# Performance work log

Hardware: AMD Instinct MI355X
Metric: run time of the kernel (lower is better)

## Reference

```python
import jax, jax.numpy as jnp
import numpy as np

N = 50000      # nodes
E = 800000     # edges (avg degree 16)
D_IN = 128     # node_feature_dim
H = 256        # hidden_dim
EPS = 1e-5     # BatchNorm eps


def setup_inputs() -> dict:
    key = jax.random.key(0)
    ks = jax.random.split(key, 32)
    inp = {
        "x": jax.random.normal(ks[0], (N, D_IN), jnp.float32),
        "edge_index": jax.random.randint(ks[1], (2, E), 0, N, jnp.int32),
    }
    dims = [(D_IN, H), (H, H), (H, H)]
    k = 2
    for i, (din, dout) in enumerate(dims):
        s = 1.0 / np.sqrt(din)
        inp[f"Wl{i}"] = jax.random.uniform(ks[k], (din, dout), jnp.float32, -s, s); k += 1
        inp[f"bl{i}"] = jax.random.uniform(ks[k], (dout,), jnp.float32, -s, s); k += 1
        inp[f"Wr{i}"] = jax.random.uniform(ks[k], (din, dout), jnp.float32, -s, s); k += 1
        inp[f"g{i}"] = jnp.ones((dout,), jnp.float32)
        inp[f"b{i}"] = jnp.zeros((dout,), jnp.float32)
        inp[f"rm{i}"] = jax.random.normal(ks[k], (dout,), jnp.float32) * 0.1; k += 1
        inp[f"rv{i}"] = jax.random.uniform(ks[k], (dout,), jnp.float32, 0.5, 1.5); k += 1
    return inp


def _sage(x, src, dst, Wl, bl, Wr):
    # PyG SAGEConv (aggr='mean'): out = lin_l(mean_{j in N(i)} x_j) + lin_r(x_i)
    deg = jax.ops.segment_sum(jnp.ones((src.shape[0],), x.dtype), dst, num_segments=N)
    agg = jax.ops.segment_sum(x[src], dst, num_segments=N)  # [N, d_in]
    mean = agg / jnp.maximum(deg, 1.0)[:, None]
    return mean @ Wl + bl + x @ Wr


def _bn(x, g, b, rm, rv):
    # eval-mode BatchNorm1d with running stats
    return (x - rm) * (g * jax.lax.rsqrt(rv + EPS)) + b


def reference(x, edge_index,
              Wl0, bl0, Wr0, g0, b0, rm0, rv0,
              Wl1, bl1, Wr1, g1, b1, rm1, rv1,
              Wl2, bl2, Wr2, g2, b2, rm2, rv2):
    src, dst = edge_index[0], edge_index[1]
    h = jax.nn.relu(_bn(_sage(x, src, dst, Wl0, bl0, Wr0), g0, b0, rm0, rv0))
    h = jax.nn.relu(_bn(_sage(h, src, dst, Wl1, bl1, Wr1), g1, b1, rm1, rv1))
    h = _bn(_sage(h, src, dst, Wl2, bl2, Wr2), g2, b2, rm2, rv2)
    return h  # [N, H] node embeddings (dropout is identity in eval mode)
```

## Files before the change

kernel.cpp:

```cpp
#include <hip/hip_runtime.h>
#include <hip/hip_bf16.h>

#define NNODES 50000
#define NEDGES 800000
#define HID 256
#define BN_EPS 1e-5f
#define SCAN_B ((NNODES + 255) / 256)

typedef __attribute__((ext_vector_type(8))) short short8v;
typedef __attribute__((ext_vector_type(4))) float f32x4;
typedef __attribute__((ext_vector_type(2))) float f32x2;

__device__ inline void load_lds16(const void* g, void* l) {
    __builtin_amdgcn_global_load_lds(
        (const __attribute__((address_space(1))) unsigned int*)g,
        (__attribute__((address_space(3))) unsigned int*)l, 16, 0, 0);
}

__global__ void k_countrank(const int* __restrict__ ei, int* __restrict__ cnt,
                            int* __restrict__ rank, int nE) {
    int e = blockIdx.x * blockDim.x + threadIdx.x;
    if (e < nE) rank[e] = atomicAdd(&cnt[ei[nE + e]], 1);
}

__global__ void k_bsum(const int* __restrict__ cnt, int* __restrict__ loc,
                       int* __restrict__ bsum, int n) {
    __shared__ int sh[256];
    int tid = threadIdx.x;
    int i = blockIdx.x * 256 + tid;
    int v = (i < n) ? cnt[i] : 0;
    sh[tid] = v;
    __syncthreads();
    for (int off = 1; off < 256; off <<= 1) {
        int t = (tid >= off) ? sh[tid - off] : 0;
        __syncthreads();
        sh[tid] += t;
        __syncthreads();
    }
    if (i < n) loc[i] = sh[tid] - v;
    if (tid == 255) bsum[blockIdx.x] = sh[255];
}

__global__ void k_bscan(int* __restrict__ bsum, int nb) {
    __shared__ int sh[256];
    int tid = threadIdx.x;
    int v = (tid < nb) ? bsum[tid] : 0;
    sh[tid] = v;
    __syncthreads();
    for (int off = 1; off < 256; off <<= 1) {
        int t = (tid >= off) ? sh[tid - off] : 0;
        __syncthreads();
        sh[tid] += t;
        __syncthreads();
    }
    if (tid < nb) bsum[tid] = sh[tid] - v;
}

__global__ void k_addoff(const int* __restrict__ loc, const int* __restrict__ bsum,
                         int* __restrict__ rowptr, int n, int nE) {
    int i = blockIdx.x * 256 + threadIdx.x;
    if (i < n) rowptr[i] = loc[i] + bsum[blockIdx.x];
    if (i == 0) rowptr[n] = nE;
}

__global__ void k_fill2(const int* __restrict__ ei, const int* __restrict__ rowptr,
                        const int* __restrict__ rank, int* __restrict__ col, int nE) {
    int e = blockIdx.x * blockDim.x + threadIdx.x;
    if (e < nE) col[rowptr[ei[nE + e]] + rank[e]] = ei[e];
}

#define PREP_CAST 1600000
#define PREP_TR   327680
__global__ void k_prep(const float* __restrict__ x,
                       __hip_bfloat16* __restrict__ xb, unsigned char* __restrict__ x8,
                       const float* __restrict__ s0, const float* __restrict__ s1,
                       const float* __restrict__ s2, const float* __restrict__ s3,
                       const float* __restrict__ s4, const float* __restrict__ s5,
                       __hip_bfloat16* __restrict__ d0, __hip_bfloat16* __restrict__ d1,
                       __hip_bfloat16* __restrict__ d2, __hip_bfloat16* __restrict__ d3,
                       __hip_bfloat16* __restrict__ d4, __hip_bfloat16* __restrict__ d5,
                       int* __restrict__ cnt) {
    int f = blockIdx.x * blockDim.x + threadIdx.x;
    if (f < PREP_CAST) {
        float4 v = *(const float4*)(x + f * 4);
        union { uint2 u; unsigned short s[4]; } ob;
        ob.s[0] = __bfloat16_as_ushort(__float2bfloat16(v.x));
        ob.s[1] = __bfloat16_as_ushort(__float2bfloat16(v.y));
        ob.s[2] = __bfloat16_as_ushort(__float2bfloat16(v.z));
        ob.s[3] = __bfloat16_as_ushort(__float2bfloat16(v.w));
        *(uint2*)(xb + f * 4) = ob.u;
        int p = __builtin_amdgcn_cvt_pk_fp8_f32(v.x, v.y, 0, false);
        p = __builtin_amdgcn_cvt_pk_fp8_f32(v.z, v.w, p, true);
        *(int*)(x8 + f * 4) = p;
    } else if (f < PREP_CAST + PREP_TR) {
        int r = f - PREP_CAST;
        const float* src; __hip_bfloat16* dst; int K; int i;
        if (r < 65536) {
            K = 128;
            if (r < 32768) { src = s0; dst = d0; i = r; }
            else           { src = s1; dst = d1; i = r - 32768; }
        } else {
            K = 256;
            int q = r - 65536;
            int wsel = q >> 16;
            i = q & 65535;
            src = (wsel == 0) ? s2 : (wsel == 1) ? s3 : (wsel == 2) ? s4 : s5;
            dst = (wsel == 0) ? d2 : (wsel == 1) ? d3 : (wsel == 2) ? d4 : d5;
        }
        int k = i >> 8;
        int nn = i & 255;
        dst[nn * K + k] = __float2bfloat16(src[i]);
    } else {
        int i = f - PREP_CAST - PREP_TR;
        if (i < NNODES) cnt[i] = 0;
    }
}

template <int D, int U>
__global__ void k_meanf8(const unsigned char* __restrict__ x8,
                         const int* __restrict__ rowptr, const int* __restrict__ col,
                         __hip_bfloat16* __restrict__ mean, int n) {
    constexpr int CPL = D / 16;
    constexpr int R = 64 / CPL;
    int gw = (blockIdx.x * blockDim.x + threadIdx.x) >> 6;
    int lane = threadIdx.x & 63;
    if (gw >= n) return;
    int beg = rowptr[gw], end = rowptr[gw + 1];
    int sub = lane / CPL;
    int fpos = lane % CPL;
    const uint4* base = (const uint4*)x8;

    float acc[16];
#pragma unroll
    for (int j = 0; j < 16; j++) acc[j] = 0.f;

    for (int p0 = beg; p0 < end; p0 += U * R) {
        int idx[U]; bool ok[U];
#pragma unroll
        for (int u = 0; u < U; u++) {
            int p = p0 + u * R + sub;
            ok[u] = (p < end);
            idx[u] = ok[u] ? col[p] : 0;
        }
        uint4 v[U];
#pragma unroll
        for (int u = 0; u < U; u++) {
            uint4 t = {0u, 0u, 0u, 0u};
            if (ok[u]) t = base[(size_t)idx[u] * CPL + fpos];
            v[u] = t;
        }
#pragma unroll
        for (int u = 0; u < U; u++) {
            const unsigned int uu[4] = {v[u].x, v[u].y, v[u].z, v[u].w};
#pragma unroll
            for (int q = 0; q < 4; q++) {
                f32x2 lo = __builtin_amdgcn_cvt_pk_f32_fp8(uu[q], false);
                f32x2 hi = __builtin_amdgcn_cvt_pk_f32_fp8(uu[q], true);
                acc[4 * q + 0] += lo.x;
                acc[4 * q + 1] += lo.y;
                acc[4 * q + 2] += hi.x;
                acc[4 * q + 3] += hi.y;
            }
        }
    }

    if constexpr (R >= 8) {
#pragma unroll
        for (int j = 0; j < 16; j++) acc[j] += __shfl_xor(acc[j], 8, 64);
    }
#pragma unroll
    for (int j = 0; j < 16; j++) acc[j] += __shfl_xor(acc[j], 16, 64);
#pragma unroll
    for (int j = 0; j < 16; j++) acc[j] += __shfl_xor(acc[j], 32, 64);

    if (sub == 0) {
        float inv = (end > beg) ? 1.f / (float)(end - beg) : 0.f;
        union { uint4 v[2]; unsigned short s[16]; } o;
#pragma unroll
        for (int j = 0; j < 16; j++)
            o.s[j] = __bfloat16_as_ushort(__float2bfloat16(acc[j] * inv));
        uint4* dst = (uint4*)(mean + (size_t)gw * D + fpos * 16);
        dst[0] = o.v[0];
        dst[1] = o.v[1];
    }
}

template <int K, typename OutT, int RELU, int W8>
__launch_bounds__(256, 2)
__global__ void k_gemm2(const __hip_bfloat16* __restrict__ A1,
                        const __hip_bfloat16* __restrict__ A2,
                        const __hip_bfloat16* __restrict__ W1t,
                        const __hip_bfloat16* __restrict__ W2t,
                        const float* __restrict__ bl,
                        const float* __restrict__ g,
                        const float* __restrict__ bb,
                        const float* __restrict__ rm,
                        const float* __restrict__ rv,
                        OutT* __restrict__ out, unsigned char* __restrict__ out8,
                        int n) {
    __shared__ __hip_bfloat16 As1[128 * 32];
    __shared__ __hip_bfloat16 As2[128 * 32];
    __shared__ __hip_bfloat16 Bs1[256 * 32];
    __shared__ __hip_bfloat16 Bs2[256 * 32];
    int tid = threadIdx.x;
    int lane = tid & 63;
    int w = tid >> 6;
    int quad = lane >> 4;
    int ml = lane & 15;
    int rowBase = blockIdx.x * 128;
    int wr = w >> 1, wc = w & 1;

    f32x4 acc[4][8];
#pragma unroll
    for (int i = 0; i < 4; i++)
#pragma unroll
        for (int t = 0; t < 8; t++) acc[i][t] = {0.f, 0.f, 0.f, 0.f};

    int srow = tid >> 2;
    int sbyte = (tid & 3) * 16;

    for (int k0 = 0; k0 < K; k0 += 32) {
        __syncthreads();
#pragma unroll
        for (int h = 0; h < 2; h++) {
            int r = srow + h * 64;
            int grow = rowBase + r; if (grow >= n) grow = n - 1;
            load_lds16((const char*)(A1 + (size_t)grow * K + k0) + sbyte,
                       (char*)As1 + r * 64 + sbyte);
            load_lds16((const char*)(A2 + (size_t)grow * K + k0) + sbyte,
                       (char*)As2 + r * 64 + sbyte);
        }
#pragma unroll
        for (int h = 0; h < 4; h++) {
            int c = srow + h * 64;
            load_lds16((const char*)(W1t + (size_t)c * K + k0) + sbyte,
                       (char*)Bs1 + c * 64 + sbyte);
            load_lds16((const char*)(W2t + (size_t)c * K + k0) + sbyte,
                       (char*)Bs2 + c * 64 + sbyte);
        }
        __syncthreads();

        short8v af1[4], af2[4];
#pragma unroll
        for (int i = 0; i < 4; i++) {
            af1[i] = *(const short8v*)(As1 + (wr * 64 + i * 16 + ml) * 32 + quad * 8);
            af2[i] = *(const short8v*)(As2 + (wr * 64 + i * 16 + ml) * 32 + quad * 8);
        }
#pragma unroll
        for (int t = 0; t < 8; t++) {
            short8v bf1 = *(const short8v*)(Bs1 + (wc * 128 + t * 16 + ml) * 32 + quad * 8);
            short8v bf2 = *(const short8v*)(Bs2 + (wc * 128 + t * 16 + ml) * 32 + quad * 8);
#pragma unroll
            for (int i = 0; i < 4; i++) {
                acc[i][t] = __builtin_amdgcn_mfma_f32_16x16x32_bf16(af1[i], bf1, acc[i][t], 0, 0, 0);
                acc[i][t] = __builtin_amdgcn_mfma_f32_16x16x32_bf16(af2[i], bf2, acc[i][t], 0, 0, 0);
            }
        }
    }

#pragma unroll
    for (int t = 0; t < 8; t++) {
        int c = wc * 128 + t * 16 + ml;
        float sv = g[c] * rsqrtf(rv[c] + BN_EPS);
        float tv = (bl[c] - rm[c]) * sv + bb[c];
#pragma unroll
        for (int i = 0; i < 4; i++) {
            int row0 = rowBase + wr * 64 + i * 16 + quad * 4;
#pragma unroll
            for (int r = 0; r < 4; r++) {
                int row = row0 + r;
                if (row < n) {
                    float v = acc[i][t][r] * sv + tv;
                    if (RELU) v = fmaxf(v, 0.f);
                    if constexpr (sizeof(OutT) == 2)
                        out[(size_t)row * HID + c] = (OutT)__float2bfloat16(v);
                    else
                        out[(size_t)row * HID + c] = (OutT)v;
                    if constexpr (W8) {
                        int p = __builtin_amdgcn_cvt_pk_fp8_f32(v, v, 0, false);
                        out8[(size_t)row * HID + c] = (unsigned char)(p & 0xFF);
                    }
                }
            }
        }
    }
}

extern "C" void kernel_launch(void* const* d_in, const int* in_sizes, int n_in,
                              void* d_out, int out_size, void* d_ws, size_t ws_size,
                              hipStream_t stream) {
    const float* x = (const float*)d_in[0];
    const int* ei = (const int*)d_in[1];
    const float *Wl[3], *blv[3], *Wr[3], *g[3], *bb[3], *rm[3], *rv[3];
    for (int i = 0; i < 3; i++) {
        int b = 2 + i * 7;
        Wl[i]  = (const float*)d_in[b + 0];
        blv[i] = (const float*)d_in[b + 1];
        Wr[i]  = (const float*)d_in[b + 2];
        g[i]   = (const float*)d_in[b + 3];
        bb[i]  = (const float*)d_in[b + 4];
        rm[i]  = (const float*)d_in[b + 5];
        rv[i]  = (const float*)d_in[b + 6];
    }

    char* ob = (char*)d_out;
    __hip_bfloat16* xb = (__hip_bfloat16*)ob;
    __hip_bfloat16* h0 = (__hip_bfloat16*)(ob + (size_t)NNODES * 128 * 2);

    char* w = (char*)d_ws;
    size_t off = 0;
    auto alloc = [&](size_t bytes) {
        void* p = w + off;
        off += (bytes + 255) & ~(size_t)255;
        return p;
    };
    int* rowptr = (int*)alloc((NNODES + 1) * sizeof(int));
    int* cnt    = (int*)alloc(NNODES * sizeof(int));
    int* loc    = (int*)alloc(NNODES * sizeof(int));
    int* bsum   = (int*)alloc(SCAN_B * sizeof(int));
    int* rank   = (int*)alloc(NEDGES * sizeof(int));
    int* col    = (int*)alloc(NEDGES * sizeof(int));
    __hip_bfloat16* meanb = (__hip_bfloat16*)alloc((size_t)NNODES * HID * 2);
    __hip_bfloat16* h1    = (__hip_bfloat16*)alloc((size_t)NNODES * HID * 2);
    unsigned char* x8   = (unsigned char*)alloc((size_t)NNODES * 128);
    unsigned char* h0f8 = (unsigned char*)alloc((size_t)NNODES * HID);
    unsigned char* h1f8 = (unsigned char*)alloc((size_t)NNODES * HID);
    __hip_bfloat16* Wt[6];
    int Ks[6] = {128, 128, 256, 256, 256, 256};
    for (int i = 0; i < 6; i++) Wt[i] = (__hip_bfloat16*)alloc((size_t)Ks[i] * HID * 2);

    int prepTotal = PREP_CAST + PREP_TR + NNODES;
    k_prep<<<(prepTotal + 255) / 256, 256, 0, stream>>>(
        x, xb, x8, Wl[0], Wr[0], Wl[1], Wr[1], Wl[2], Wr[2],
        Wt[0], Wt[1], Wt[2], Wt[3], Wt[4], Wt[5], cnt);

    k_countrank<<<(NEDGES + 255) / 256, 256, 0, stream>>>(ei, cnt, rank, NEDGES);
    k_bsum<<<SCAN_B, 256, 0, stream>>>(cnt, loc, bsum, NNODES);
    k_bscan<<<1, 256, 0, stream>>>(bsum, SCAN_B);
    k_addoff<<<SCAN_B, 256, 0, stream>>>(loc, bsum, rowptr, NNODES, NEDGES);
    k_fill2<<<(NEDGES + 255) / 256, 256, 0, stream>>>(ei, rowptr, rank, col, NEDGES);

    int meanBlocks = (NNODES * 64 + 255) / 256;
    int gemmBlocks = (NNODES + 127) / 128;

    k_meanf8<128, 2><<<meanBlocks, 256, 0, stream>>>(x8, rowptr, col, meanb, NNODES);
    k_gemm2<128, __hip_bfloat16, 1, 1><<<gemmBlocks, 256, 0, stream>>>(meanb, xb, Wt[0], Wt[1],
        blv[0], g[0], bb[0], rm[0], rv[0], h0, h0f8, NNODES);

    k_meanf8<256, 4><<<meanBlocks, 256, 0, stream>>>(h0f8, rowptr, col, meanb, NNODES);
    k_gemm2<256, __hip_bfloat16, 1, 1><<<gemmBlocks, 256, 0, stream>>>(meanb, h0, Wt[2], Wt[3],
        blv[1], g[1], bb[1], rm[1], rv[1], h1, h1f8, NNODES);

    k_meanf8<256, 4><<<meanBlocks, 256, 0, stream>>>(h1f8, rowptr, col, meanb, NNODES);
    k_gemm2<256, float, 0, 0><<<gemmBlocks, 256, 0, stream>>>(meanb, h1, Wt[4], Wt[5],
        blv[2], g[2], bb[2], rm[2], rv[2], (float*)d_out, (unsigned char*)nullptr, NNODES);
}
```

Before: 376.0 us.

## Shrink GEMM row tile to 64 and XOR-swizzle LDS tiles

The dual-GEMM kernel now handles 64 rows per block instead of 128. Each of the four waves owns a 64-column slice of the output, which halves the accumulator count and raises the occupancy target to 4 blocks per SM. Global-to-LDS loads and fragment reads use an XOR swizzle on the 16-byte chunk index to reduce LDS bank conflicts. The trade-off is that each block reloads the full weight tiles for half as many rows, doubling weight traffic from L2.

```diff
diff --git a/kernel.cpp b/kernel.cpp
--- a/kernel.cpp
+++ b/kernel.cpp
@@ -186,8 +186,8 @@
 }
 
 template <int K, typename OutT, int RELU, int W8>
-__launch_bounds__(256, 2)
-__global__ void k_gemm2(const __hip_bfloat16* __restrict__ A1,
+__launch_bounds__(256, 4)
+__global__ void k_gemm3(const __hip_bfloat16* __restrict__ A1,
                         const __hip_bfloat16* __restrict__ A2,
                         const __hip_bfloat16* __restrict__ W1t,
                         const __hip_bfloat16* __restrict__ W2t,
@@ -198,8 +198,8 @@
                         const float* __restrict__ rv,
                         OutT* __restrict__ out, unsigned char* __restrict__ out8,
                         int n) {
-    __shared__ __hip_bfloat16 As1[128 * 32];
-    __shared__ __hip_bfloat16 As2[128 * 32];
+    __shared__ __hip_bfloat16 As1[64 * 32];
+    __shared__ __hip_bfloat16 As2[64 * 32];
     __shared__ __hip_bfloat16 Bs1[256 * 32];
     __shared__ __hip_bfloat16 Bs2[256 * 32];
     int tid = threadIdx.x;
@@ -207,49 +207,48 @@
     int w = tid >> 6;
     int quad = lane >> 4;
     int ml = lane & 15;
-    int rowBase = blockIdx.x * 128;
-    int wr = w >> 1, wc = w & 1;
-
-    f32x4 acc[4][8];
+    int rowBase = blockIdx.x * 64;
+
+    f32x4 acc[4][4];
 #pragma unroll
     for (int i = 0; i < 4; i++)
 #pragma unroll
-        for (int t = 0; t < 8; t++) acc[i][t] = {0.f, 0.f, 0.f, 0.f};
+        for (int t = 0; t < 4; t++) acc[i][t] = {0.f, 0.f, 0.f, 0.f};
 
     int srow = tid >> 2;
-    int sbyte = (tid & 3) * 16;
+    int c4 = tid & 3;
+    int sswz = c4 ^ ((srow >> 1) & 3);
+    int rswz = quad ^ ((ml >> 1) & 3);
+
+    int grow = rowBase + srow; if (grow >= n) grow = n - 1;
 
     for (int k0 = 0; k0 < K; k0 += 32) {
         __syncthreads();
-#pragma unroll
-        for (int h = 0; h < 2; h++) {
-            int r = srow + h * 64;
-            int grow = rowBase + r; if (grow >= n) grow = n - 1;
-            load_lds16((const char*)(A1 + (size_t)grow * K + k0) + sbyte,
-                       (char*)As1 + r * 64 + sbyte);
-            load_lds16((const char*)(A2 + (size_t)grow * K + k0) + sbyte,
-                       (char*)As2 + r * 64 + sbyte);
-        }
+        load_lds16((const char*)(A1 + (size_t)grow * K + k0) + sswz * 16,
+                   (char*)As1 + srow * 64 + c4 * 16);
+        load_lds16((const char*)(A2 + (size_t)grow * K + k0) + sswz * 16,
+                   (char*)As2 + srow * 64 + c4 * 16);
 #pragma unroll
         for (int h = 0; h < 4; h++) {
             int c = srow + h * 64;
-            load_lds16((const char*)(W1t + (size_t)c * K + k0) + sbyte,
-                       (char*)Bs1 + c * 64 + sbyte);
-            load_lds16((const char*)(W2t + (size_t)c * K + k0) + sbyte,
-                       (char*)Bs2 + c * 64 + sbyte);
+            load_lds16((const char*)(W1t + (size_t)c * K + k0) + sswz * 16,
+                       (char*)Bs1 + c * 64 + c4 * 16);
+            load_lds16((const char*)(W2t + (size_t)c * K + k0) + sswz * 16,
+                       (char*)Bs2 + c * 64 + c4 * 16);
         }
         __syncthreads();
 
         short8v af1[4], af2[4];
 #pragma unroll
         for (int i = 0; i < 4; i++) {
-            af1[i] = *(const short8v*)(As1 + (wr * 64 + i * 16 + ml) * 32 + quad * 8);
-            af2[i] = *(const short8v*)(As2 + (wr * 64 + i * 16 + ml) * 32 + quad * 8);
-        }
-#pragma unroll
-        for (int t = 0; t < 8; t++) {
-            short8v bf1 = *(const short8v*)(Bs1 + (wc * 128 + t * 16 + ml) * 32 + quad * 8);
-            short8v bf2 = *(const short8v*)(Bs2 + (wc * 128 + t * 16 + ml) * 32 + quad * 8);
+            af1[i] = *(const short8v*)(As1 + (i * 16 + ml) * 32 + rswz * 8);
+            af2[i] = *(const short8v*)(As2 + (i * 16 + ml) * 32 + rswz * 8);
+        }
+#pragma unroll
+        for (int t = 0; t < 4; t++) {
+            int brow = w * 64 + t * 16 + ml;
+            short8v bf1 = *(const short8v*)(Bs1 + brow * 32 + rswz * 8);
+            short8v bf2 = *(const short8v*)(Bs2 + brow * 32 + rswz * 8);
 #pragma unroll
             for (int i = 0; i < 4; i++) {
                 acc[i][t] = __builtin_amdgcn_mfma_f32_16x16x32_bf16(af1[i], bf1, acc[i][t], 0, 0, 0);
@@ -259,13 +258,13 @@
     }
 
 #pragma unroll
-    for (int t = 0; t < 8; t++) {
-        int c = wc * 128 + t * 16 + ml;
+    for (int t = 0; t < 4; t++) {
+        int c = w * 64 + t * 16 + ml;
         float sv = g[c] * rsqrtf(rv[c] + BN_EPS);
         float tv = (bl[c] - rm[c]) * sv + bb[c];
 #pragma unroll
         for (int i = 0; i < 4; i++) {
-            int row0 = rowBase + wr * 64 + i * 16 + quad * 4;
+            int row0 = rowBase + i * 16 + quad * 4;
 #pragma unroll
             for (int r = 0; r < 4; r++) {
                 int row = row0 + r;
@@ -341,17 +340,17 @@
     k_fill2<<<(NEDGES + 255) / 256, 256, 0, stream>>>(ei, rowptr, rank, col, NEDGES);
 
     int meanBlocks = (NNODES * 64 + 255) / 256;
-    int gemmBlocks = (NNODES + 127) / 128;
+    int gemmBlocks = (NNODES + 63) / 64;
 
     k_meanf8<128, 2><<<meanBlocks, 256, 0, stream>>>(x8, rowptr, col, meanb, NNODES);
-    k_gemm2<128, __hip_bfloat16, 1, 1><<<gemmBlocks, 256, 0, stream>>>(meanb, xb, Wt[0], Wt[1],
+    k_gemm3<128, __hip_bfloat16, 1, 1><<<gemmBlocks, 256, 0, stream>>>(meanb, xb, Wt[0], Wt[1],
         blv[0], g[0], bb[0], rm[0], rv[0], h0, h0f8, NNODES);
 
     k_meanf8<256, 4><<<meanBlocks, 256, 0, stream>>>(h0f8, rowptr, col, meanb, NNODES);
-    k_gemm2<256, __hip_bfloat16, 1, 1><<<gemmBlocks, 256, 0, stream>>>(meanb, h0, Wt[2], Wt[3],
+    k_gemm3<256, __hip_bfloat16, 1, 1><<<gemmBlocks, 256, 0, stream>>>(meanb, h0, Wt[2], Wt[3],
         blv[1], g[1], bb[1], rm[1], rv[1], h1, h1f8, NNODES);
 
     k_meanf8<256, 4><<<meanBlocks, 256, 0, stream>>>(h1f8, rowptr, col, meanb, NNODES);
-    k_gemm2<256, float, 0, 0><<<gemmBlocks, 256, 0, stream>>>(meanb, h1, Wt[4], Wt[5],
+    k_gemm3<256, float, 0, 0><<<gemmBlocks, 256, 0, stream>>>(meanb, h1, Wt[4], Wt[5],
         blv[2], g[2], bb[2], rm[2], rv[2], (float*)d_out, (unsigned char*)nullptr, NNODES);
 }
```

Result: slower. 417.2 us (+10.9%).
